# Performance work log

Hardware: AMD Instinct MI355X
Metric: run time of the kernel (lower is better)

The kernel has to match this reference:

```python
import jax, jax.numpy as jnp
import numpy as np


def setup_inputs() -> dict:
    key = jax.random.key(0)
    R = 7  # pos_bias_radius
    # Learned parameter: biases of shape [(2R+1)]*3. (Initialized to zeros in the
    # original; use random values so correctness checks are meaningful.)
    biases = jax.random.normal(key, (2 * R + 1, 2 * R + 1, 2 * R + 1), dtype=jnp.float32)
    return {"biases": biases, "H": 20, "W": 20, "D": 20}


def reference(biases, H, W, D):
    # Equivalent math to the original scatter-into-padded-tensor-then-slice:
    # pos_biases[h1,w1,d1,h2,w2,d2] = biases[h2-h1+R, w2-w1+R, d2-d1+R]
    #                                 if all offsets within [-R, R], else 0.
    # Computed as a direct masked gather; never materializes the padded tensor.
    R = (biases.shape[0] - 1) // 2
    S = 2 * R  # max valid index into biases along each axis

    def rel(n):
        idx = jnp.arange(n)
        d = idx[:, None] - idx[None, :] + R  # [n, n], value h1? no: (h2 - h1) below
        return d

    # d*[i2, i1] convention: we want h2 - h1 + R -> build as col - row transposed.
    dh = jnp.arange(H)[None, :] - jnp.arange(H)[:, None] + R  # [H(h1), H(h2)]
    dw = jnp.arange(W)[None, :] - jnp.arange(W)[:, None] + R  # [W, W]
    dd = jnp.arange(D)[None, :] - jnp.arange(D)[:, None] + R  # [D, D]

    mh, mw, md = (0 <= dh) & (dh <= S), (0 <= dw) & (dw <= S), (0 <= dd) & (dd <= S)
    dh_c, dw_c, dd_c = jnp.clip(dh, 0, S), jnp.clip(dw, 0, S), jnp.clip(dd, 0, S)

    # Broadcast-gather to [H, W, D, H, W, D]
    ih = dh_c[:, None, None, :, None, None]
    iw = dw_c[None, :, None, None, :, None]
    id_ = dd_c[None, None, :, None, None, :]
    vals = biases[ih, iw, id_]  # [H, W, D, H, W, D]

    mask = (mh[:, None, None, :, None, None]
            & mw[None, :, None, None, :, None]
            & md[None, None, :, None, None, :])
    pos_biases = jnp.where(mask, vals, jnp.zeros((), dtype=biases.dtype))
    N = H * W * D
    return pos_biases.reshape(N, N)
```

## Files before the change

### kernel.cpp

```cpp
#include <hip/hip_runtime.h>


constexpr int R  = 7;
constexpr int S1 = 2 * R + 1;
constexpr int SB = S1 * S1 * S1;

constexpr int H = 20, W = 20, D = 20;
constexpr int N = H * W * D;

__global__ __launch_bounds__(256)
void SlidingPosBiases3D_kernel(const float* __restrict__ biases,
                               float* __restrict__ out) {
    const int row = blockIdx.x;
    const int d = row % D;
    const int w = (row / D) % W;
    const int h = row / (W * D);

    __shared__ float sb[SB];
    for (int i = threadIdx.x; i < SB; i += blockDim.x)
        sb[i] = biases[i];
    __syncthreads();

    float4* __restrict__ orow = (float4*)(out + (size_t)row * N);
    const int nvec = N / 4;

    for (int v = threadIdx.x; v < nvec; v += blockDim.x) {
        const int col = v * 4;
        const int d0  = col % D;
        const int rem = col / D;
        const int wp  = rem % W;
        const int hp  = rem / W;

        const int ih = hp - h + R;
        const int iw = wp - w + R;

        float4 val = make_float4(0.f, 0.f, 0.f, 0.f);
        if ((unsigned)ih < (unsigned)S1 && (unsigned)iw < (unsigned)S1) {
            const int base = ih * (S1 * S1) + iw * S1;
            float* vp = (float*)&val;
            #pragma unroll
            for (int k = 0; k < 4; ++k) {
                const int id = d0 + k - d + R;
                vp[k] = ((unsigned)id < (unsigned)S1) ? sb[base + id] : 0.f;
            }
        }
        orow[v] = val;
    }
}

extern "C" void kernel_launch(void* const* d_in, const int* in_sizes, int n_in,
                              void* d_out, int out_size, void* d_ws, size_t ws_size,
                              hipStream_t stream) {
    const float* biases = (const float*)d_in[0];
    float* out = (float*)d_out;
    SlidingPosBiases3D_kernel<<<N, 256, 0, stream>>>(biases, out);
}
```

Before: 46.03 us.

## Process four rows per block sharing bias window, use nontemporal stores

Each block now writes four consecutive output rows that share h and w, gathering a 7-element bias window once and emitting shifted float4 slices for each row. Stores use nontemporal builtins to avoid polluting caches on a purely streaming write. This cuts index arithmetic and shared-memory loads per output element and reduces grid size fourfold, at the cost of fewer blocks and more registers per thread.

```diff
diff --git a/kernel.cpp b/kernel.cpp
--- a/kernel.cpp
+++ b/kernel.cpp
@@ -1,5 +1,7 @@
 #include <hip/hip_runtime.h>
 
+
+typedef float v4f __attribute__((ext_vector_type(4)));
 
 constexpr int R  = 7;
 constexpr int S1 = 2 * R + 1;
@@ -7,24 +9,27 @@
 
 constexpr int H = 20, W = 20, D = 20;
 constexpr int N = H * W * D;
+constexpr int NV = N / 4;
+constexpr int RPB = 4;
+constexpr int NBLK = N / RPB;
 
 __global__ __launch_bounds__(256)
 void SlidingPosBiases3D_kernel(const float* __restrict__ biases,
                                float* __restrict__ out) {
-    const int row = blockIdx.x;
-    const int d = row % D;
-    const int w = (row / D) % W;
-    const int h = row / (W * D);
-
     __shared__ float sb[SB];
-    for (int i = threadIdx.x; i < SB; i += blockDim.x)
+    for (int i = threadIdx.x; i < SB; i += 256)
         sb[i] = biases[i];
     __syncthreads();
 
-    float4* __restrict__ orow = (float4*)(out + (size_t)row * N);
-    const int nvec = N / 4;
+    const int row0  = blockIdx.x * RPB;
+    const int dbase = row0 % D;
+    const int hw    = row0 / D;
+    const int w     = hw % W;
+    const int h     = hw / W;
 
-    for (int v = threadIdx.x; v < nvec; v += blockDim.x) {
+    float* __restrict__ obase = out + (size_t)row0 * N;
+
+    for (int v = threadIdx.x; v < NV; v += 256) {
         const int col = v * 4;
         const int d0  = col % D;
         const int rem = col / D;
@@ -33,18 +38,25 @@
 
         const int ih = hp - h + R;
         const int iw = wp - w + R;
+        const bool ok = ((unsigned)ih < (unsigned)S1) & ((unsigned)iw < (unsigned)S1);
+        const int base = ih * (S1 * S1) + iw * S1;
+        const int e    = d0 - dbase + R;
 
-        float4 val = make_float4(0.f, 0.f, 0.f, 0.f);
-        if ((unsigned)ih < (unsigned)S1 && (unsigned)iw < (unsigned)S1) {
-            const int base = ih * (S1 * S1) + iw * S1;
-            float* vp = (float*)&val;
-            #pragma unroll
-            for (int k = 0; k < 4; ++k) {
-                const int id = d0 + k - d + R;
-                vp[k] = ((unsigned)id < (unsigned)S1) ? sb[base + id] : 0.f;
-            }
+        float t[7];
+        #pragma unroll
+        for (int j = 0; j < 7; ++j) {
+            const int id = e - 3 + j;
+            const bool m = ok & ((unsigned)id < (unsigned)S1);
+            int idc = id < 0 ? 0 : (id > S1 - 1 ? S1 - 1 : id);
+            const int addr = ok ? base + idc : 0;
+            t[j] = m ? sb[addr] : 0.f;
         }
-        orow[v] = val;
+
+        #pragma unroll
+        for (int r = 0; r < RPB; ++r) {
+            v4f val = { t[3 - r], t[4 - r], t[5 - r], t[6 - r] };
+            __builtin_nontemporal_store(val, (v4f*)(obase + (size_t)r * N) + v);
+        }
     }
 }
 
@@ -53,5 +65,5 @@
                               hipStream_t stream) {
     const float* biases = (const float*)d_in[0];
     float* out = (float*)d_out;
-    SlidingPosBiases3D_kernel<<<N, 256, 0, stream>>>(biases, out);
+    SlidingPosBiases3D_kernel<<<NBLK, 256, 0, stream>>>(biases, out);
 }
```

Measured after the change: 55.69 us. 1.21x slower.
